# Kernel optimization log

Hardware: AMD Instinct MI355X
Metric: run time of the kernel (lower is better)

The kernel has to match this reference:

```python
import jax, jax.numpy as jnp
import numpy as np

N = 500_000      # lidar points
ODOM = 3
ACT = 5


def setup_inputs() -> dict:
    key = jax.random.key(0)
    ks = jax.random.split(key, 40)
    f32 = jnp.float32
    def rn(k, shape, s=0.05):
        return jax.random.normal(k, shape, dtype=f32) * s
    d = {
        "x": rn(ks[0], (3 + 2 * N,), 1.0),
        "hx": rn(ks[1], (1, 128), 1.0),
        "cx": rn(ks[2], (1, 128), 1.0),
        # PointNet: conv1d k=1 == per-point matmul
        "c1w": rn(ks[3], (16, 2)),  "c1b": rn(ks[4], (16,)),
        "c2w": rn(ks[5], (32, 16)), "c2b": rn(ks[6], (32,)),
        "c3w": rn(ks[7], (64, 32)), "c3b": rn(ks[8], (64,)),
        "fcw": rn(ks[9], (64, 64)), "fcb": rn(ks[10], (64,)),
        # odom net 3->8->8
        "o1w": rn(ks[11], (8, 3)),  "o1b": rn(ks[12], (8,)),
        "o2w": rn(ks[13], (8, 8)),  "o2b": rn(ks[14], (8,)),
        # prior 72->128
        "pw": rn(ks[15], (128, 72)), "pb": rn(ks[16], (128,)),
        # LSTMCell(128,128): torch gate order i,f,g,o
        "wih": rn(ks[17], (512, 128)), "whh": rn(ks[18], (512, 128)),
        "bih": rn(ks[19], (512,)),     "bhh": rn(ks[20], (512,)),
        # post 128->64->64
        "q1w": rn(ks[21], (64, 128)), "q1b": rn(ks[22], (64,)),
        "q2w": rn(ks[23], (64, 64)),  "q2b": rn(ks[24], (64,)),
        # actor 64->16->ACT, softmax
        "aw1": rn(ks[25], (16, 64)), "ab1": rn(ks[26], (16,)),
        "aw2": rn(ks[27], (ACT, 16)), "ab2": rn(ks[28], (ACT,)),
        # critics 64->16->1
        "ciw1": rn(ks[29], (16, 64)), "cib1": rn(ks[30], (16,)),
        "ciw2": rn(ks[31], (1, 16)),  "cib2": rn(ks[32], (1,)),
        "cew1": rn(ks[33], (16, 64)), "ceb1": rn(ks[34], (16,)),
        "cew2": rn(ks[35], (1, 16)),  "ceb2": rn(ks[36], (1,)),
    }
    return d


def reference(x, hx, cx,
              c1w, c1b, c2w, c2b, c3w, c3b, fcw, fcb,
              o1w, o1b, o2w, o2b, pw, pb,
              wih, whh, bih, bhh,
              q1w, q1b, q2w, q2b,
              aw1, ab1, aw2, ab2,
              ciw1, cib1, ciw2, cib2,
              cew1, ceb1, cew2, ceb2):
    odom = x[:ODOM]                       # (3,)
    pts = x[ODOM:].reshape(2, N)          # (2, N)
    # PointNet: three 1x1 convs (per-point matmuls) + global max + fc
    h = jax.nn.relu(c1w @ pts + c1b[:, None])   # (16, N)
    h = jax.nn.relu(c2w @ h + c2b[:, None])     # (32, N)
    h = jax.nn.relu(c3w @ h + c3b[:, None])     # (64, N)
    feat = jnp.max(h, axis=1)                    # (64,)
    obs = fcw @ feat + fcb                       # (64,)
    # odom net
    pose = jax.nn.relu(o2w @ jax.nn.sigmoid(o1w @ odom + o1b) + o2b)  # (8,)
    # prior MLP
    z = jax.nn.relu(pw @ jnp.concatenate([obs, pose]) + pb)           # (128,)
    # LSTMCell (torch semantics, gate order i,f,g,o)
    gates = z @ wih.T + bih + hx[0] @ whh.T + bhh                     # (512,)
    i, f, g, o = jnp.split(gates, 4)
    c_new = jax.nn.sigmoid(f) * cx[0] + jax.nn.sigmoid(i) * jnp.tanh(g)
    h_new = jax.nn.sigmoid(o) * jnp.tanh(c_new)                       # (128,)
    hx2 = h_new[None, :]
    cx2 = c_new[None, :]
    # post MLP
    zp = jax.nn.relu(q1w @ h_new + q1b)
    zp = jax.nn.relu(q2w @ zp + q2b)                                  # (64,)
    # heads
    actor = jax.nn.softmax(aw2 @ jax.nn.relu(aw1 @ zp + ab1) + ab2)   # (ACT,)
    ci = ciw2 @ jax.nn.relu(ciw1 @ zp + cib1) + cib2                  # (1,)
    ce = cew2 @ jax.nn.relu(cew1 @ zp + ceb1) + ceb2                  # (1,)
    return (actor, ci, ce, hx2, cx2, pose)
```

## Files before the change

### kernel.cpp

```cpp
#include <hip/hip_runtime.h>

#define NBLK 1024

#define WS_Z    0
#define WS_GHH  128
#define WS_HNEW 640
#define WS_ZP1  768
#define WS_FEAT 840
#define WS_POSE 904
#define WS_OBS  912
#define WS_PART 1024

typedef __attribute__((ext_vector_type(8))) short bf16x8;
typedef __attribute__((ext_vector_type(4))) float f32x4;

union U4 { unsigned int u[4]; bf16x8 v; };

static __device__ __forceinline__ unsigned int pack_bf16(float lo, float hi) {
    return (__float_as_uint(hi) & 0xFFFF0000u) | (__float_as_uint(lo) >> 16);
}

__global__ __launch_bounds__(64) void prep_kernel(unsigned int* __restrict__ g)
{
    g[threadIdx.x & 63] = 0u;
}

__global__ __launch_bounds__(256) void encoder_kernel(
    const float* __restrict__ x,
    const float* __restrict__ c1w, const float* __restrict__ c1b,
    const float* __restrict__ c2w, const float* __restrict__ c2b,
    const float* __restrict__ c3w,
    float* __restrict__ ws, int N, int use_atomic)
{
    __shared__ float sW1x[16], sW1y[16], sB1s[16];
    __shared__ float sW2[512], sB2[32];
    __shared__ float sW3[2048];
    __shared__ unsigned int sh2[4 * 272];
    __shared__ float wred[4 * 64];

    int t = threadIdx.x;
    if (t < 16) { sW1x[t] = c1w[2 * t]; sW1y[t] = c1w[2 * t + 1]; sB1s[t] = c1b[t]; }
    if (t < 32) sB2[t] = c2b[t];
    for (int i = t; i < 512; i += 256)  sW2[i] = c2w[i];
    for (int i = t; i < 2048; i += 256) sW3[i] = c3w[i];
    __syncthreads();

    const int lane = t & 63, wid = t >> 6;
    const int n16 = lane & 15, q = lane >> 4;

    bf16x8 a2[2];
#pragma unroll
    for (int tt = 0; tt < 2; ++tt)
#pragma unroll
        for (int j = 0; j < 8; ++j) {
            int k = q * 8 + j;
            float w = (k < 16) ? sW2[(tt * 16 + n16) * 16 + k] : 0.0f;
            a2[tt][j] = (short)(__float_as_uint(w) >> 16);
        }
    bf16x8 a3[4];
#pragma unroll
    for (int tt = 0; tt < 4; ++tt)
#pragma unroll
        for (int j = 0; j < 8; ++j) {
            float w = sW3[(tt * 16 + n16) * 32 + q * 8 + j];
            a3[tt][j] = (short)(__float_as_uint(w) >> 16);
        }
    float w1x[8], w1y[8], b1v[8];
#pragma unroll
    for (int j = 0; j < 8; ++j) {
        int k = q * 8 + j;
        if (k < 16) { w1x[j] = sW1x[k]; w1y[j] = sW1y[k]; b1v[j] = sB1s[k]; }
        else        { w1x[j] = 0.f;     w1y[j] = 0.f;     b1v[j] = 0.f; }
    }
    float b2a[4], b2b[4];
#pragma unroll
    for (int r = 0; r < 4; ++r) { b2a[r] = sB2[q * 4 + r]; b2b[r] = sB2[16 + q * 4 + r]; }

    float vmax[16];
#pragma unroll
    for (int i = 0; i < 16; ++i) vmax[i] = -INFINITY;

    unsigned int* hb = sh2 + wid * 272;
    const int WPG = NBLK * 4;
    const int gw = blockIdx.x * 4 + wid;
    const int niter = (N + WPG * 16 - 1) / (WPG * 16);

    int p = gw * 16 + n16; if (p >= N) p = N - 1;
    float px = x[3 + p], py = x[3 + N + p];

#pragma unroll 1
    for (int it = 0; it < niter; ++it) {
        float cpx = px, cpy = py;
        if (it + 1 < niter) {
            int pn = ((it + 1) * WPG + gw) * 16 + n16;
            if (pn >= N) pn = N - 1;
            px = x[3 + pn]; py = x[3 + N + pn];
        }

        unsigned int h1d0 = 0, h1d1 = 0, h1d2 = 0, h1d3 = 0;
        if (q < 2) {
            float h0 = fmaxf(fmaf(w1x[0], cpx, fmaf(w1y[0], cpy, b1v[0])), 0.f);
            float h1 = fmaxf(fmaf(w1x[1], cpx, fmaf(w1y[1], cpy, b1v[1])), 0.f);
            float h2 = fmaxf(fmaf(w1x[2], cpx, fmaf(w1y[2], cpy, b1v[2])), 0.f);
            float h3 = fmaxf(fmaf(w1x[3], cpx, fmaf(w1y[3], cpy, b1v[3])), 0.f);
            float h4 = fmaxf(fmaf(w1x[4], cpx, fmaf(w1y[4], cpy, b1v[4])), 0.f);
            float h5 = fmaxf(fmaf(w1x[5], cpx, fmaf(w1y[5], cpy, b1v[5])), 0.f);
            float h6 = fmaxf(fmaf(w1x[6], cpx, fmaf(w1y[6], cpy, b1v[6])), 0.f);
            float h7 = fmaxf(fmaf(w1x[7], cpx, fmaf(w1y[7], cpy, b1v[7])), 0.f);
            h1d0 = pack_bf16(h0, h1); h1d1 = pack_bf16(h2, h3);
            h1d2 = pack_bf16(h4, h5); h1d3 = pack_bf16(h6, h7);
        }
        U4 bu; bu.u[0] = h1d0; bu.u[1] = h1d1; bu.u[2] = h1d2; bu.u[3] = h1d3;

        f32x4 z4 = {0.f, 0.f, 0.f, 0.f};
        f32x4 acc2a = __builtin_amdgcn_mfma_f32_16x16x32_bf16(a2[0], bu.v, z4, 0, 0, 0);
        f32x4 acc2b = __builtin_amdgcn_mfma_f32_16x16x32_bf16(a2[1], bu.v, z4, 0, 0, 0);

        unsigned int base = (unsigned int)(n16 * 17);
        hb[base + 2 * q]     = pack_bf16(fmaxf(acc2a[0] + b2a[0], 0.f),
                                         fmaxf(acc2a[1] + b2a[1], 0.f));
        hb[base + 2 * q + 1] = pack_bf16(fmaxf(acc2a[2] + b2a[2], 0.f),
                                         fmaxf(acc2a[3] + b2a[3], 0.f));
        hb[base + 8 + 2 * q] = pack_bf16(fmaxf(acc2b[0] + b2b[0], 0.f),
                                         fmaxf(acc2b[1] + b2b[1], 0.f));
        hb[base + 9 + 2 * q] = pack_bf16(fmaxf(acc2b[2] + b2b[2], 0.f),
                                         fmaxf(acc2b[3] + b2b[3], 0.f));
        __builtin_amdgcn_s_waitcnt(0xc07f);
        U4 ru;
        ru.u[0] = hb[base + 4 * q];     ru.u[1] = hb[base + 4 * q + 1];
        ru.u[2] = hb[base + 4 * q + 2]; ru.u[3] = hb[base + 4 * q + 3];

        f32x4 o0 = __builtin_amdgcn_mfma_f32_16x16x32_bf16(a3[0], ru.v, z4, 0, 0, 0);
        f32x4 o1 = __builtin_amdgcn_mfma_f32_16x16x32_bf16(a3[1], ru.v, z4, 0, 0, 0);
        f32x4 o2 = __builtin_amdgcn_mfma_f32_16x16x32_bf16(a3[2], ru.v, z4, 0, 0, 0);
        f32x4 o3 = __builtin_amdgcn_mfma_f32_16x16x32_bf16(a3[3], ru.v, z4, 0, 0, 0);
#pragma unroll
        for (int r = 0; r < 4; ++r) {
            vmax[r]      = fmaxf(vmax[r],      o0[r]);
            vmax[4 + r]  = fmaxf(vmax[4 + r],  o1[r]);
            vmax[8 + r]  = fmaxf(vmax[8 + r],  o2[r]);
            vmax[12 + r] = fmaxf(vmax[12 + r], o3[r]);
        }
    }

#pragma unroll
    for (int i = 0; i < 16; ++i) {
        float v = vmax[i];
        v = fmaxf(v, __shfl_xor(v, 1, 64));
        v = fmaxf(v, __shfl_xor(v, 2, 64));
        v = fmaxf(v, __shfl_xor(v, 4, 64));
        v = fmaxf(v, __shfl_xor(v, 8, 64));
        vmax[i] = v;
    }
    if (n16 == 0) {
#pragma unroll
        for (int tt = 0; tt < 4; ++tt)
#pragma unroll
            for (int r = 0; r < 4; ++r)
                wred[wid * 64 + tt * 16 + q * 4 + r] = vmax[tt * 4 + r];
    }
    __syncthreads();
    if (t < 64) {
        float m = fmaxf(fmaxf(wred[t], wred[64 + t]),
                        fmaxf(wred[128 + t], wred[192 + t]));
        if (use_atomic) {
            unsigned int b = __float_as_uint(m);
            unsigned int e = (b & 0x80000000u) ? ~b : (b | 0x80000000u);
            atomicMax((unsigned int*)ws + WS_PART + t, e);
        } else {
            ws[WS_PART + blockIdx.x * 64 + t] = m;
        }
    }
}

__global__ __launch_bounds__(256) void tail_k1(
    const float* __restrict__ x,   const float* __restrict__ hx,
    const float* __restrict__ whh, const float* __restrict__ bhh,
    const float* __restrict__ c3b,
    const float* __restrict__ o1w, const float* __restrict__ o1b,
    const float* __restrict__ o2w, const float* __restrict__ o2b,
    float* __restrict__ ws, float* __restrict__ out, int use_atomic)
{
    const int b = blockIdx.x, t = threadIdx.x;
    __shared__ float shx[128], sig8L[8], odomL[3];

    if (t < 128) shx[t] = hx[t];
    __syncthreads();

    {
        const int rl = t >> 3, sub = t & 7;
        const int gr = (rl >> 3) * 128 + b * 8 + (rl & 7);
        const float4* w4 = (const float4*)(whh + (size_t)gr * 128) + sub * 4;
        float s = 0.0f;
#pragma unroll
        for (int j = 0; j < 4; j++) {
            float4 w = w4[j];
            int k = sub * 16 + 4 * j;
            s = fmaf(w.x, shx[k], fmaf(w.y, shx[k + 1],
                fmaf(w.z, shx[k + 2], fmaf(w.w, shx[k + 3], s))));
        }
        s += __shfl_xor(s, 1, 64); s += __shfl_xor(s, 2, 64); s += __shfl_xor(s, 4, 64);
        if (sub == 0) ws[WS_GHH + gr] = bhh[gr] + s;
    }

    if (!use_atomic) {
        int w = t >> 6, lane = t & 63;
        int c = b * 4 + w;
        float m = -INFINITY;
        const float* part = ws + WS_PART;
#pragma unroll 4
        for (int j = 0; j < NBLK / 64; j++)
            m = fmaxf(m, part[(lane * (NBLK / 64) + j) * 64 + c]);
#pragma unroll
        for (int off = 32; off > 0; off >>= 1)
            m = fmaxf(m, __shfl_xor(m, off, 64));
        if (lane == 0) ws[WS_FEAT + c] = fmaxf(m + c3b[c], 0.0f);
    } else if (b == 0 && t >= 64 && t < 128) {
        int c = t - 64;
        unsigned int u = ((unsigned int*)ws)[WS_PART + c];
        unsigned int bb = (u & 0x80000000u) ? (u ^ 0x80000000u) : ~u;
        ws[WS_FEAT + c] = fmaxf(__uint_as_float(bb) + c3b[c], 0.0f);
    }

    if (b == 0) {
        if (t < 3) odomL[t] = x[t];
        __syncthreads();
        if (t < 8) {
            float s = o1b[t];
            for (int k = 0; k < 3; k++) s = fmaf(o1w[t * 3 + k], odomL[k], s);
            sig8L[t] = 1.0f / (1.0f + expf(-s));
        }
        __syncthreads();
        if (t < 8) {
            float s = o2b[t];
            for (int k = 0; k < 8; k++) s = fmaf(o2w[t * 8 + k], sig8L[k], s);
            float pv = fmaxf(s, 0.0f);
            ws[WS_POSE + t] = pv;
            out[263 + t] = pv;
        }
    }
}

__global__ __launch_bounds__(256) void tail_k2a(
    const float* __restrict__ fcw, const float* __restrict__ fcb,
    float* __restrict__ ws)
{
    const int b = blockIdx.x, t = threadIdx.x;
    __shared__ float featL[64];
    if (t < 64) featL[t] = ws[WS_FEAT + t];
    __syncthreads();
    int row = b * 4 + (t >> 6), lane = t & 63;
    float s = fcw[(size_t)row * 64 + lane] * featL[lane];
#pragma unroll
    for (int off = 32; off > 0; off >>= 1) s += __shfl_xor(s, off, 64);
    if (lane == 0) ws[WS_OBS + row] = s + fcb[row];
}

__global__ __launch_bounds__(256) void tail_k2b(
    const float* __restrict__ pw, const float* __restrict__ pb,
    float* __restrict__ ws)
{
    const int b = blockIdx.x, t = threadIdx.x;
    __shared__ float inL[72];
    if (t < 64) inL[t] = ws[WS_OBS + t];
    else if (t < 72) inL[t] = ws[WS_POSE + t - 64];
    __syncthreads();
    int rowl = t >> 5, l32 = t & 31;
    int row = b * 8 + rowl;
    const float* wr = pw + (size_t)row * 72;
    float s = wr[l32] * inL[l32] + wr[l32 + 32] * inL[l32 + 32];
    if (l32 < 8) s = fmaf(wr[l32 + 64], inL[l32 + 64], s);
    s += __shfl_xor(s, 1, 64); s += __shfl_xor(s, 2, 64);
    s += __shfl_xor(s, 4, 64); s += __shfl_xor(s, 8, 64); s += __shfl_xor(s, 16, 64);
    if (l32 == 0) ws[WS_Z + row] = fmaxf(s + pb[row], 0.0f);
}

__global__ __launch_bounds__(256) void tail_k3(
    const float* __restrict__ wih, const float* __restrict__ bih,
    const float* __restrict__ cx,
    float* __restrict__ ws, float* __restrict__ out)
{
    const int b = blockIdx.x, t = threadIdx.x;
    __shared__ float zL[128], lg[32];
    if (t < 128) zL[t] = ws[WS_Z + t];
    __syncthreads();

    const int rl = t >> 3, sub = t & 7;
    const int gr = (rl >> 3) * 128 + b * 8 + (rl & 7);
    const float4* w4 = (const float4*)(wih + (size_t)gr * 128) + sub * 4;
    float s = 0.0f;
#pragma unroll
    for (int j = 0; j < 4; j++) {
        float4 w = w4[j];
        int k = sub * 16 + 4 * j;
        s = fmaf(w.x, zL[k], fmaf(w.y, zL[k + 1],
            fmaf(w.z, zL[k + 2], fmaf(w.w, zL[k + 3], s))));
    }
    s += __shfl_xor(s, 1, 64); s += __shfl_xor(s, 2, 64); s += __shfl_xor(s, 4, 64);
    if (sub == 0) lg[rl] = ws[WS_GHH + gr] + bih[gr] + s;
    __syncthreads();

    if (t < 8) {
        int c = b * 8 + t;
        float gI = lg[t], gF = lg[8 + t], gG = lg[16 + t], gO = lg[24 + t];
        float ig = 1.0f / (1.0f + expf(-gI));
        float fg = 1.0f / (1.0f + expf(-gF));
        float gg = tanhf(gG);
        float og = 1.0f / (1.0f + expf(-gO));
        float cn = fg * cx[c] + ig * gg;
        float hn = og * tanhf(cn);
        out[7 + c] = hn;
        out[135 + c] = cn;
        ws[WS_HNEW + c] = hn;
    }
}

__global__ __launch_bounds__(256) void tail_k4(
    const float* __restrict__ q1w, const float* __restrict__ q1b,
    float* __restrict__ ws)
{
    const int b = blockIdx.x, t = threadIdx.x;
    __shared__ float hnL[128];
    if (t < 128) hnL[t] = ws[WS_HNEW + t];
    __syncthreads();
    int row = b * 4 + (t >> 6), lane = t & 63;
    const float* wr = q1w + (size_t)row * 128;
    float s = fmaf(wr[2 * lane], hnL[2 * lane], wr[2 * lane + 1] * hnL[2 * lane + 1]);
#pragma unroll
    for (int off = 32; off > 0; off >>= 1) s += __shfl_xor(s, off, 64);
    if (lane == 0) ws[WS_ZP1 + row] = fmaxf(s + q1b[row], 0.0f);
}

__global__ __launch_bounds__(256) void tail_k5(
    const float* __restrict__ q2w, const float* __restrict__ q2b,
    const float* __restrict__ aw1, const float* __restrict__ ab1,
    const float* __restrict__ aw2, const float* __restrict__ ab2,
    const float* __restrict__ ciw1, const float* __restrict__ cib1,
    const float* __restrict__ ciw2, const float* __restrict__ cib2,
    const float* __restrict__ cew1, const float* __restrict__ ceb1,
    const float* __restrict__ cew2, const float* __restrict__ ceb2,
    const float* __restrict__ ws, float* __restrict__ out)
{
    const int t = threadIdx.x;
    __shared__ float zp1L[64], zp2L[64], a1s[16], cih[16], ceh[16], logits[5];
    if (t < 64) zp1L[t] = ws[WS_ZP1 + t];
    __syncthreads();
    if (t < 64) {
        float s = q2b[t];
        const float4* q4 = (const float4*)(q2w + (size_t)t * 64);
        for (int qq = 0; qq < 16; qq++) {
            float4 w = q4[qq];
            s = fmaf(w.x, zp1L[4 * qq], fmaf(w.y, zp1L[4 * qq + 1],
                fmaf(w.z, zp1L[4 * qq + 2], fmaf(w.w, zp1L[4 * qq + 3], s))));
        }
        zp2L[t] = fmaxf(s, 0.0f);
    }
    __syncthreads();
    if (t < 16) {
        float s = ab1[t];
        for (int k = 0; k < 64; k++) s = fmaf(aw1[t * 64 + k], zp2L[k], s);
        a1s[t] = fmaxf(s, 0.0f);
    } else if (t < 32) {
        int r = t - 16;
        float s = cib1[r];
        for (int k = 0; k < 64; k++) s = fmaf(ciw1[r * 64 + k], zp2L[k], s);
        cih[r] = fmaxf(s, 0.0f);
    } else if (t < 48) {
        int r = t - 32;
        float s = ceb1[r];
        for (int k = 0; k < 64; k++) s = fmaf(cew1[r * 64 + k], zp2L[k], s);
        ceh[r] = fmaxf(s, 0.0f);
    }
    __syncthreads();
    if (t < 5) {
        float s = ab2[t];
        for (int k = 0; k < 16; k++) s = fmaf(aw2[t * 16 + k], a1s[k], s);
        logits[t] = s;
    } else if (t == 5) {
        float s = cib2[0];
        for (int k = 0; k < 16; k++) s = fmaf(ciw2[k], cih[k], s);
        out[5] = s;
    } else if (t == 6) {
        float s = ceb2[0];
        for (int k = 0; k < 16; k++) s = fmaf(cew2[k], ceh[k], s);
        out[6] = s;
    }
    __syncthreads();
    if (t == 0) {
        float m = logits[0];
        for (int i = 1; i < 5; i++) m = fmaxf(m, logits[i]);
        float e[5], s = 0.0f;
        for (int i = 0; i < 5; i++) { e[i] = expf(logits[i] - m); s += e[i]; }
        for (int i = 0; i < 5; i++) out[i] = e[i] / s;
    }
}

extern "C" void kernel_launch(void* const* d_in, const int* in_sizes, int n_in,
                              void* d_out, int out_size, void* d_ws, size_t ws_size,
                              hipStream_t stream)
{
    const float* x    = (const float*)d_in[0];
    const float* hx   = (const float*)d_in[1];
    const float* cx   = (const float*)d_in[2];
    const float* c1w  = (const float*)d_in[3];
    const float* c1b  = (const float*)d_in[4];
    const float* c2w  = (const float*)d_in[5];
    const float* c2b  = (const float*)d_in[6];
    const float* c3w  = (const float*)d_in[7];
    const float* c3b  = (const float*)d_in[8];
    const float* fcw  = (const float*)d_in[9];
    const float* fcb  = (const float*)d_in[10];
    const float* o1w  = (const float*)d_in[11];
    const float* o1b  = (const float*)d_in[12];
    const float* o2w  = (const float*)d_in[13];
    const float* o2b  = (const float*)d_in[14];
    const float* pw   = (const float*)d_in[15];
    const float* pb   = (const float*)d_in[16];
    const float* wih  = (const float*)d_in[17];
    const float* whh  = (const float*)d_in[18];
    const float* bih  = (const float*)d_in[19];
    const float* bhh  = (const float*)d_in[20];
    const float* q1w  = (const float*)d_in[21];
    const float* q1b  = (const float*)d_in[22];
    const float* q2w  = (const float*)d_in[23];
    const float* q2b  = (const float*)d_in[24];
    const float* aw1  = (const float*)d_in[25];
    const float* ab1  = (const float*)d_in[26];
    const float* aw2  = (const float*)d_in[27];
    const float* ab2  = (const float*)d_in[28];
    const float* ciw1 = (const float*)d_in[29];
    const float* cib1 = (const float*)d_in[30];
    const float* ciw2 = (const float*)d_in[31];
    const float* cib2 = (const float*)d_in[32];
    const float* cew1 = (const float*)d_in[33];
    const float* ceb1 = (const float*)d_in[34];
    const float* cew2 = (const float*)d_in[35];
    const float* ceb2 = (const float*)d_in[36];

    int N = (in_sizes[0] - 3) / 2;
    size_t need = (size_t)(1024 + NBLK * 64) * 4;
    int use_atomic = (ws_size < need) ? 1 : 0;
    float* ws = (float*)d_ws;
    float* out = (float*)d_out;

    if (use_atomic)
        prep_kernel<<<1, 64, 0, stream>>>((unsigned int*)d_ws + WS_PART);
    encoder_kernel<<<NBLK, 256, 0, stream>>>(x, c1w, c1b, c2w, c2b, c3w,
                                             ws, N, use_atomic);
    tail_k1<<<16, 256, 0, stream>>>(x, hx, whh, bhh, c3b, o1w, o1b, o2w, o2b,
                                    ws, out, use_atomic);
    tail_k2a<<<16, 256, 0, stream>>>(fcw, fcb, ws);
    tail_k2b<<<16, 256, 0, stream>>>(pw, pb, ws);
    tail_k3<<<16, 256, 0, stream>>>(wih, bih, cx, ws, out);
    tail_k4<<<16, 256, 0, stream>>>(q1w, q1b, ws);
    tail_k5<<<1, 256, 0, stream>>>(q2w, q2b, aw1, ab1, aw2, ab2, ciw1, cib1,
                                   ciw2, cib2, cew1, ceb1, cew2, ceb2, ws, out);
}
```

Before: 160.8 us.

## Fuse tail MLP/LSTM kernels into one kernel with grid-wide spin barriers

Replaces six small sequential tail kernels with a single 16-block kernel that passes intermediates through workspace using agent-scope atomic stores/loads and a software grid barrier. Single-block stages (fc, prior MLP, post MLP heads) run in block 0 with intermediates kept in shared memory. This removes several kernel launch gaps on a latency-bound tail, at the cost of spin-wait barriers that rely on all 16 blocks being co-resident.

```diff
diff --git a/kernel.cpp b/kernel.cpp
--- a/kernel.cpp
+++ b/kernel.cpp
@@ -7,9 +7,10 @@
 #define WS_HNEW 640
 #define WS_ZP1  768
 #define WS_FEAT 840
-#define WS_POSE 904
-#define WS_OBS  912
+#define WS_BAR  992
 #define WS_PART 1024
+
+#define NTB 16
 
 typedef __attribute__((ext_vector_type(8))) short bf16x8;
 typedef __attribute__((ext_vector_type(4))) float f32x4;
@@ -18,6 +19,23 @@
 
 static __device__ __forceinline__ unsigned int pack_bf16(float lo, float hi) {
     return (__float_as_uint(hi) & 0xFFFF0000u) | (__float_as_uint(lo) >> 16);
+}
+
+static __device__ __forceinline__ void ag_store(float* p, float v) {
+    __hip_atomic_store(p, v, __ATOMIC_RELEASE, __HIP_MEMORY_SCOPE_AGENT);
+}
+static __device__ __forceinline__ float ag_load(const float* p) {
+    return __hip_atomic_load(p, __ATOMIC_ACQUIRE, __HIP_MEMORY_SCOPE_AGENT);
+}
+
+static __device__ __forceinline__ void bar_sync(unsigned int* bar, int idx) {
+    __syncthreads();
+    if (threadIdx.x == 0) {
+        __hip_atomic_fetch_add(&bar[idx], 1u, __ATOMIC_ACQ_REL, __HIP_MEMORY_SCOPE_AGENT);
+        while (__hip_atomic_load(&bar[idx], __ATOMIC_ACQUIRE,
+                                 __HIP_MEMORY_SCOPE_AGENT) < NTB) {}
+    }
+    __syncthreads();
 }
 
 __global__ __launch_bounds__(64) void prep_kernel(unsigned int* __restrict__ g)
@@ -39,6 +57,7 @@
     __shared__ float wred[4 * 64];
 
     int t = threadIdx.x;
+    if (blockIdx.x == 0 && t < 8) ((unsigned int*)ws)[WS_BAR + t] = 0u;
     if (t < 16) { sW1x[t] = c1w[2 * t]; sW1y[t] = c1w[2 * t + 1]; sB1s[t] = c1b[t]; }
     if (t < 32) sB2[t] = c2b[t];
     for (int i = t; i < 512; i += 256)  sW2[i] = c2w[i];
@@ -173,20 +192,34 @@
     }
 }
 
-__global__ __launch_bounds__(256) void tail_k1(
+__global__ __launch_bounds__(256) void tail_fused(
     const float* __restrict__ x,   const float* __restrict__ hx,
-    const float* __restrict__ whh, const float* __restrict__ bhh,
-    const float* __restrict__ c3b,
+    const float* __restrict__ cx,  const float* __restrict__ c3b,
+    const float* __restrict__ fcw, const float* __restrict__ fcb,
     const float* __restrict__ o1w, const float* __restrict__ o1b,
     const float* __restrict__ o2w, const float* __restrict__ o2b,
+    const float* __restrict__ pw,  const float* __restrict__ pb,
+    const float* __restrict__ wih, const float* __restrict__ whh,
+    const float* __restrict__ bih, const float* __restrict__ bhh,
+    const float* __restrict__ q1w, const float* __restrict__ q1b,
+    const float* __restrict__ q2w, const float* __restrict__ q2b,
+    const float* __restrict__ aw1, const float* __restrict__ ab1,
+    const float* __restrict__ aw2, const float* __restrict__ ab2,
+    const float* __restrict__ ciw1, const float* __restrict__ cib1,
+    const float* __restrict__ ciw2, const float* __restrict__ cib2,
+    const float* __restrict__ cew1, const float* __restrict__ ceb1,
+    const float* __restrict__ cew2, const float* __restrict__ ceb2,
     float* __restrict__ ws, float* __restrict__ out, int use_atomic)
 {
     const int b = blockIdx.x, t = threadIdx.x;
-    __shared__ float shx[128], sig8L[8], odomL[3];
+    unsigned int* bar = (unsigned int*)ws + WS_BAR;
+    __shared__ float shx[128], inL[72], zL[128], lg[32], hnL[128];
+    __shared__ float featL[64], obsL[64], zp1L[64], zp2L[64];
+    __shared__ float sig8L[8], odomL[3], poseL[8];
+    __shared__ float a1s[16], cih[16], ceh[16], logits[5];
 
     if (t < 128) shx[t] = hx[t];
     __syncthreads();
-
     {
         const int rl = t >> 3, sub = t & 7;
         const int gr = (rl >> 3) * 128 + b * 8 + (rl & 7);
@@ -202,7 +235,6 @@
         s += __shfl_xor(s, 1, 64); s += __shfl_xor(s, 2, 64); s += __shfl_xor(s, 4, 64);
         if (sub == 0) ws[WS_GHH + gr] = bhh[gr] + s;
     }
-
     if (!use_atomic) {
         int w = t >> 6, lane = t & 63;
         int c = b * 4 + w;
@@ -214,14 +246,13 @@
 #pragma unroll
         for (int off = 32; off > 0; off >>= 1)
             m = fmaxf(m, __shfl_xor(m, off, 64));
-        if (lane == 0) ws[WS_FEAT + c] = fmaxf(m + c3b[c], 0.0f);
-    } else if (b == 0 && t >= 64 && t < 128) {
-        int c = t - 64;
+        if (lane == 0) ag_store(&ws[WS_FEAT + c], fmaxf(m + c3b[c], 0.0f));
+    } else if (b == 0 && t >= 128 && t < 192) {
+        int c = t - 128;
         unsigned int u = ((unsigned int*)ws)[WS_PART + c];
         unsigned int bb = (u & 0x80000000u) ? (u ^ 0x80000000u) : ~u;
-        ws[WS_FEAT + c] = fmaxf(__uint_as_float(bb) + c3b[c], 0.0f);
-    }
-
+        ag_store(&ws[WS_FEAT + c], fmaxf(__uint_as_float(bb) + c3b[c], 0.0f));
+    }
     if (b == 0) {
         if (t < 3) odomL[t] = x[t];
         __syncthreads();
@@ -235,71 +266,68 @@
             float s = o2b[t];
             for (int k = 0; k < 8; k++) s = fmaf(o2w[t * 8 + k], sig8L[k], s);
             float pv = fmaxf(s, 0.0f);
-            ws[WS_POSE + t] = pv;
+            poseL[t] = pv;
             out[263 + t] = pv;
         }
     }
-}
-
-__global__ __launch_bounds__(256) void tail_k2a(
-    const float* __restrict__ fcw, const float* __restrict__ fcb,
-    float* __restrict__ ws)
-{
-    const int b = blockIdx.x, t = threadIdx.x;
-    __shared__ float featL[64];
-    if (t < 64) featL[t] = ws[WS_FEAT + t];
-    __syncthreads();
-    int row = b * 4 + (t >> 6), lane = t & 63;
-    float s = fcw[(size_t)row * 64 + lane] * featL[lane];
-#pragma unroll
-    for (int off = 32; off > 0; off >>= 1) s += __shfl_xor(s, off, 64);
-    if (lane == 0) ws[WS_OBS + row] = s + fcb[row];
-}
-
-__global__ __launch_bounds__(256) void tail_k2b(
-    const float* __restrict__ pw, const float* __restrict__ pb,
-    float* __restrict__ ws)
-{
-    const int b = blockIdx.x, t = threadIdx.x;
-    __shared__ float inL[72];
-    if (t < 64) inL[t] = ws[WS_OBS + t];
-    else if (t < 72) inL[t] = ws[WS_POSE + t - 64];
-    __syncthreads();
-    int rowl = t >> 5, l32 = t & 31;
-    int row = b * 8 + rowl;
-    const float* wr = pw + (size_t)row * 72;
-    float s = wr[l32] * inL[l32] + wr[l32 + 32] * inL[l32 + 32];
-    if (l32 < 8) s = fmaf(wr[l32 + 64], inL[l32 + 64], s);
-    s += __shfl_xor(s, 1, 64); s += __shfl_xor(s, 2, 64);
-    s += __shfl_xor(s, 4, 64); s += __shfl_xor(s, 8, 64); s += __shfl_xor(s, 16, 64);
-    if (l32 == 0) ws[WS_Z + row] = fmaxf(s + pb[row], 0.0f);
-}
-
-__global__ __launch_bounds__(256) void tail_k3(
-    const float* __restrict__ wih, const float* __restrict__ bih,
-    const float* __restrict__ cx,
-    float* __restrict__ ws, float* __restrict__ out)
-{
-    const int b = blockIdx.x, t = threadIdx.x;
-    __shared__ float zL[128], lg[32];
-    if (t < 128) zL[t] = ws[WS_Z + t];
-    __syncthreads();
-
-    const int rl = t >> 3, sub = t & 7;
-    const int gr = (rl >> 3) * 128 + b * 8 + (rl & 7);
-    const float4* w4 = (const float4*)(wih + (size_t)gr * 128) + sub * 4;
-    float s = 0.0f;
-#pragma unroll
-    for (int j = 0; j < 4; j++) {
-        float4 w = w4[j];
-        int k = sub * 16 + 4 * j;
-        s = fmaf(w.x, zL[k], fmaf(w.y, zL[k + 1],
-            fmaf(w.z, zL[k + 2], fmaf(w.w, zL[k + 3], s))));
-    }
-    s += __shfl_xor(s, 1, 64); s += __shfl_xor(s, 2, 64); s += __shfl_xor(s, 4, 64);
-    if (sub == 0) lg[rl] = ws[WS_GHH + gr] + bih[gr] + s;
-    __syncthreads();
-
+    bar_sync(bar, 0);
+
+    if (b == 0) {
+        if (t < 64) featL[t] = ag_load(&ws[WS_FEAT + t]);
+        __syncthreads();
+        {
+            int row = t >> 2, sub = t & 3;
+            const float4* f4 = (const float4*)(fcw + (size_t)row * 64) + sub * 4;
+            float s = 0.0f;
+#pragma unroll
+            for (int j = 0; j < 4; j++) {
+                float4 w = f4[j];
+                int k = sub * 16 + 4 * j;
+                s = fmaf(w.x, featL[k], fmaf(w.y, featL[k + 1],
+                    fmaf(w.z, featL[k + 2], fmaf(w.w, featL[k + 3], s))));
+            }
+            s += __shfl_xor(s, 1, 64); s += __shfl_xor(s, 2, 64);
+            if (sub == 0) obsL[row] = s + fcb[row];
+        }
+        __syncthreads();
+        if (t < 64) inL[t] = obsL[t];
+        else if (t < 72) inL[t] = poseL[t - 64];
+        __syncthreads();
+        {
+            int row = t >> 1, sub = t & 1;
+            const float4* p4 = (const float4*)(pw + (size_t)row * 72) + sub * 9;
+            float s = 0.0f;
+#pragma unroll
+            for (int j = 0; j < 9; j++) {
+                float4 w = p4[j];
+                int k = sub * 36 + 4 * j;
+                s = fmaf(w.x, inL[k], fmaf(w.y, inL[k + 1],
+                    fmaf(w.z, inL[k + 2], fmaf(w.w, inL[k + 3], s))));
+            }
+            s += __shfl_xor(s, 1, 64);
+            if (sub == 0) ag_store(&ws[WS_Z + row], fmaxf(s + pb[row], 0.0f));
+        }
+    }
+    bar_sync(bar, 1);
+
+    if (t < 128) zL[t] = ag_load(&ws[WS_Z + t]);
+    __syncthreads();
+    {
+        const int rl = t >> 3, sub = t & 7;
+        const int gr = (rl >> 3) * 128 + b * 8 + (rl & 7);
+        const float4* w4 = (const float4*)(wih + (size_t)gr * 128) + sub * 4;
+        float s = 0.0f;
+#pragma unroll
+        for (int j = 0; j < 4; j++) {
+            float4 w = w4[j];
+            int k = sub * 16 + 4 * j;
+            s = fmaf(w.x, zL[k], fmaf(w.y, zL[k + 1],
+                fmaf(w.z, zL[k + 2], fmaf(w.w, zL[k + 3], s))));
+        }
+        s += __shfl_xor(s, 1, 64); s += __shfl_xor(s, 2, 64); s += __shfl_xor(s, 4, 64);
+        if (sub == 0) lg[rl] = ws[WS_GHH + gr] + bih[gr] + s;
+    }
+    __syncthreads();
     if (t < 8) {
         int c = b * 8 + t;
         float gI = lg[t], gF = lg[8 + t], gG = lg[16 + t], gO = lg[24 + t];
@@ -311,87 +339,77 @@
         float hn = og * tanhf(cn);
         out[7 + c] = hn;
         out[135 + c] = cn;
-        ws[WS_HNEW + c] = hn;
-    }
-}
-
-__global__ __launch_bounds__(256) void tail_k4(
-    const float* __restrict__ q1w, const float* __restrict__ q1b,
-    float* __restrict__ ws)
-{
-    const int b = blockIdx.x, t = threadIdx.x;
-    __shared__ float hnL[128];
-    if (t < 128) hnL[t] = ws[WS_HNEW + t];
-    __syncthreads();
-    int row = b * 4 + (t >> 6), lane = t & 63;
-    const float* wr = q1w + (size_t)row * 128;
-    float s = fmaf(wr[2 * lane], hnL[2 * lane], wr[2 * lane + 1] * hnL[2 * lane + 1]);
-#pragma unroll
-    for (int off = 32; off > 0; off >>= 1) s += __shfl_xor(s, off, 64);
-    if (lane == 0) ws[WS_ZP1 + row] = fmaxf(s + q1b[row], 0.0f);
-}
-
-__global__ __launch_bounds__(256) void tail_k5(
-    const float* __restrict__ q2w, const float* __restrict__ q2b,
-    const float* __restrict__ aw1, const float* __restrict__ ab1,
-    const float* __restrict__ aw2, const float* __restrict__ ab2,
-    const float* __restrict__ ciw1, const float* __restrict__ cib1,
-    const float* __restrict__ ciw2, const float* __restrict__ cib2,
-    const float* __restrict__ cew1, const float* __restrict__ ceb1,
-    const float* __restrict__ cew2, const float* __restrict__ ceb2,
-    const float* __restrict__ ws, float* __restrict__ out)
-{
-    const int t = threadIdx.x;
-    __shared__ float zp1L[64], zp2L[64], a1s[16], cih[16], ceh[16], logits[5];
-    if (t < 64) zp1L[t] = ws[WS_ZP1 + t];
-    __syncthreads();
-    if (t < 64) {
-        float s = q2b[t];
-        const float4* q4 = (const float4*)(q2w + (size_t)t * 64);
-        for (int qq = 0; qq < 16; qq++) {
-            float4 w = q4[qq];
-            s = fmaf(w.x, zp1L[4 * qq], fmaf(w.y, zp1L[4 * qq + 1],
-                fmaf(w.z, zp1L[4 * qq + 2], fmaf(w.w, zp1L[4 * qq + 3], s))));
-        }
-        zp2L[t] = fmaxf(s, 0.0f);
-    }
-    __syncthreads();
-    if (t < 16) {
-        float s = ab1[t];
-        for (int k = 0; k < 64; k++) s = fmaf(aw1[t * 64 + k], zp2L[k], s);
-        a1s[t] = fmaxf(s, 0.0f);
-    } else if (t < 32) {
-        int r = t - 16;
-        float s = cib1[r];
-        for (int k = 0; k < 64; k++) s = fmaf(ciw1[r * 64 + k], zp2L[k], s);
-        cih[r] = fmaxf(s, 0.0f);
-    } else if (t < 48) {
-        int r = t - 32;
-        float s = ceb1[r];
-        for (int k = 0; k < 64; k++) s = fmaf(cew1[r * 64 + k], zp2L[k], s);
-        ceh[r] = fmaxf(s, 0.0f);
-    }
-    __syncthreads();
-    if (t < 5) {
-        float s = ab2[t];
-        for (int k = 0; k < 16; k++) s = fmaf(aw2[t * 16 + k], a1s[k], s);
-        logits[t] = s;
-    } else if (t == 5) {
-        float s = cib2[0];
-        for (int k = 0; k < 16; k++) s = fmaf(ciw2[k], cih[k], s);
-        out[5] = s;
-    } else if (t == 6) {
-        float s = ceb2[0];
-        for (int k = 0; k < 16; k++) s = fmaf(cew2[k], ceh[k], s);
-        out[6] = s;
-    }
-    __syncthreads();
-    if (t == 0) {
-        float m = logits[0];
-        for (int i = 1; i < 5; i++) m = fmaxf(m, logits[i]);
-        float e[5], s = 0.0f;
-        for (int i = 0; i < 5; i++) { e[i] = expf(logits[i] - m); s += e[i]; }
-        for (int i = 0; i < 5; i++) out[i] = e[i] / s;
+        ag_store(&ws[WS_HNEW + c], hn);
+    }
+    bar_sync(bar, 2);
+
+    if (t < 128) hnL[t] = ag_load(&ws[WS_HNEW + t]);
+    __syncthreads();
+    {
+        int row = b * 4 + (t >> 6), lane = t & 63;
+        const float* wr = q1w + (size_t)row * 128;
+        float s = fmaf(wr[2 * lane], hnL[2 * lane], wr[2 * lane + 1] * hnL[2 * lane + 1]);
+#pragma unroll
+        for (int off = 32; off > 0; off >>= 1) s += __shfl_xor(s, off, 64);
+        if (lane == 0) ag_store(&ws[WS_ZP1 + row], fmaxf(s + q1b[row], 0.0f));
+    }
+    bar_sync(bar, 3);
+
+    if (b == 0) {
+        if (t < 64) zp1L[t] = ag_load(&ws[WS_ZP1 + t]);
+        __syncthreads();
+        {
+            int row = t >> 2, sub = t & 3;
+            const float4* q4 = (const float4*)(q2w + (size_t)row * 64) + sub * 4;
+            float s = 0.0f;
+#pragma unroll
+            for (int j = 0; j < 4; j++) {
+                float4 w = q4[j];
+                int k = sub * 16 + 4 * j;
+                s = fmaf(w.x, zp1L[k], fmaf(w.y, zp1L[k + 1],
+                    fmaf(w.z, zp1L[k + 2], fmaf(w.w, zp1L[k + 3], s))));
+            }
+            s += __shfl_xor(s, 1, 64); s += __shfl_xor(s, 2, 64);
+            if (sub == 0) zp2L[row] = fmaxf(s + q2b[row], 0.0f);
+        }
+        __syncthreads();
+        if (t < 16) {
+            float s = ab1[t];
+            for (int k = 0; k < 64; k++) s = fmaf(aw1[t * 64 + k], zp2L[k], s);
+            a1s[t] = fmaxf(s, 0.0f);
+        } else if (t < 32) {
+            int r = t - 16;
+            float s = cib1[r];
+            for (int k = 0; k < 64; k++) s = fmaf(ciw1[r * 64 + k], zp2L[k], s);
+            cih[r] = fmaxf(s, 0.0f);
+        } else if (t < 48) {
+            int r = t - 32;
+            float s = ceb1[r];
+            for (int k = 0; k < 64; k++) s = fmaf(cew1[r * 64 + k], zp2L[k], s);
+            ceh[r] = fmaxf(s, 0.0f);
+        }
+        __syncthreads();
+        if (t < 5) {
+            float s = ab2[t];
+            for (int k = 0; k < 16; k++) s = fmaf(aw2[t * 16 + k], a1s[k], s);
+            logits[t] = s;
+        } else if (t == 5) {
+            float s = cib2[0];
+            for (int k = 0; k < 16; k++) s = fmaf(ciw2[k], cih[k], s);
+            out[5] = s;
+        } else if (t == 6) {
+            float s = ceb2[0];
+            for (int k = 0; k < 16; k++) s = fmaf(cew2[k], ceh[k], s);
+            out[6] = s;
+        }
+        __syncthreads();
+        if (t == 0) {
+            float m = logits[0];
+            for (int i = 1; i < 5; i++) m = fmaxf(m, logits[i]);
+            float e[5], s = 0.0f;
+            for (int i = 0; i < 5; i++) { e[i] = expf(logits[i] - m); s += e[i]; }
+            for (int i = 0; i < 5; i++) out[i] = e[i] / s;
+        }
     }
 }
 
@@ -447,12 +465,9 @@
         prep_kernel<<<1, 64, 0, stream>>>((unsigned int*)d_ws + WS_PART);
     encoder_kernel<<<NBLK, 256, 0, stream>>>(x, c1w, c1b, c2w, c2b, c3w,
                                              ws, N, use_atomic);
-    tail_k1<<<16, 256, 0, stream>>>(x, hx, whh, bhh, c3b, o1w, o1b, o2w, o2b,
-                                    ws, out, use_atomic);
-    tail_k2a<<<16, 256, 0, stream>>>(fcw, fcb, ws);
-    tail_k2b<<<16, 256, 0, stream>>>(pw, pb, ws);
-    tail_k3<<<16, 256, 0, stream>>>(wih, bih, cx, ws, out);
-    tail_k4<<<16, 256, 0, stream>>>(q1w, q1b, ws);
-    tail_k5<<<1, 256, 0, stream>>>(q2w, q2b, aw1, ab1, aw2, ab2, ciw1, cib1,
-                                   ciw2, cib2, cew1, ceb1, cew2, ceb2, ws, out);
-}
+    tail_fused<<<NTB, 256, 0, stream>>>(x, hx, cx, c3b, fcw, fcb, o1w, o1b,
+                                        o2w, o2b, pw, pb, wih, whh, bih, bhh,
+                                        q1w, q1b, q2w, q2b, aw1, ab1, aw2, ab2,
+                                        ciw1, cib1, ciw2, cib2, cew1, ceb1,
+                                        cew2, ceb2, ws, out, use_atomic);
+}
```

New measurement: 159.9 us. About the same (-0.6%).
